# Kernel tuning notes

Measured on AMD Instinct MI355X. Metric: run time of the kernel, lower is better.

Reference implementation:

```python
import jax, jax.numpy as jnp
import numpy as np

B, L, E, K = 64, 1024, 256, 8  # batch, seq_len, d_model, topk (slice width)


def setup_inputs() -> dict:
    key = jax.random.key(0)
    ks = jax.random.split(key, 5)
    s = 1.0 / np.sqrt(E).astype(np.float32)
    return {
        "series": jax.random.normal(ks[0], (B, L, E), jnp.float32),
        "text_series": jax.random.normal(ks[1], (B, L, E), jnp.float32),
        "Wq": jax.random.normal(ks[2], (E, E), jnp.float32) * s,
        "bq": jnp.zeros((E,), jnp.float32),
        "Wk": jax.random.normal(ks[3], (E, E), jnp.float32) * s,
        "bk": jnp.zeros((E,), jnp.float32),
        "Wv": jax.random.normal(ks[4], (E, E), jnp.float32) * s,
        "bv": jnp.zeros((E,), jnp.float32),
    }


def reference(series, text_series, Wq, bq, Wk, bk, Wv, bv):
    Bn, Ln, En = series.shape
    scale = 1.0 / np.sqrt(En).astype(np.float32)
    # nn.Linear: x @ W.T + b
    q = series @ Wq.T + bq            # (B, L, E)
    k = text_series @ Wk.T + bk       # (B, L, E)
    v = text_series @ Wv.T + bv       # (B, L, E)
    # FFT cross-correlation along time axis
    qf = jnp.fft.rfft(q.transpose(0, 2, 1), axis=-1)  # (B, E, L//2+1)
    kf = jnp.fft.rfft(k.transpose(0, 2, 1), axis=-1)
    corr = jnp.fft.irfft(qf * jnp.conj(kf), n=Ln, axis=-1)  # (B, E, L)
    mean_value = corr.mean(axis=1)                           # (B, L)
    # torch.topk(mean over batch, seq_len) == full descending sort of lags
    idx = jnp.argsort(-mean_value.mean(axis=0))              # (L,)
    weights = mean_value[:, idx]                             # (B, L), sorted by lag score
    tmp_corr = jax.nn.softmax(weights * scale, axis=-1)      # (B, L)
    # Original builds cc = concat_i [roll(v, -idx[i], 1) * tmp_corr[:, i]] over all L lags
    # (shape (B, L, L*E)), then returns (cc[..., :K], cc[..., -K:]).
    # With K <= E those slices come solely from the first (i=0) and last (i=L-1) lag blocks.
    out1 = jnp.roll(v, -idx[0], axis=1)[..., :K] * tmp_corr[:, 0][:, None, None]
    out2 = jnp.roll(v, -idx[-1], axis=1)[..., -K:] * tmp_corr[:, -1][:, None, None]
    return (out1, out2)
```

## Files before the change

### kernel.cpp

```cpp
#include <hip/hip_runtime.h>
#include <hip/hip_bf16.h>
#include <math.h>

#define BB 64
#define LL 1024
#define EE 256
#define KK 8
#define EPB 8
#define CHUNKS (EE/EPB)

typedef __attribute__((ext_vector_type(8))) short  bfrag;
typedef __attribute__((ext_vector_type(4))) short  short4v;
typedef __attribute__((ext_vector_type(4))) float  f32x4;

#define MT_KB 10240

#define O_MHI    ((size_t)0)
#define O_MLO    ((size_t)40960)
#define O_BVAUG  ((size_t)81920)
#define O_X      ((size_t)81984)
#define O_KPT    (O_X + (size_t)16777216)
#define O_VSUB   (O_KPT + (size_t)16777216)
#define O_MV     (O_VSUB + (size_t)1048576)
#define O_STATS  (O_MV + (size_t)65536)

__device__ __forceinline__ float2 cmulf(float2 a, float2 b) {
    return make_float2(a.x * b.x - a.y * b.y, a.x * b.y + a.y * b.x);
}

__device__ __forceinline__ int PHY(int i) { return i + (i >> 4); }

__device__ __forceinline__ void splitbf(float x, unsigned short& h, unsigned short& l) {
    __hip_bfloat16 hb = __float2bfloat16(x);
    float hf = __bfloat162float(hb);
    __hip_bfloat16 lb = __float2bfloat16(x - hf);
    h = *(unsigned short*)&hb;
    l = *(unsigned short*)&lb;
}

__device__ __forceinline__ void gload16(const unsigned short* g, unsigned short* l) {
    __builtin_amdgcn_global_load_lds(
        (const __attribute__((address_space(1))) unsigned int*)g,
        (__attribute__((address_space(3))) unsigned int*)l, 16, 0, 0);
}

__device__ __forceinline__ int slot_of(int r, int kq) { return (kq + (r >> 1)) & 3; }

__global__ __launch_bounds__(256) void build_maug(
    const float* __restrict__ Wq, const float* __restrict__ Wk,
    const float* __restrict__ Wv, const float* __restrict__ bv,
    unsigned short* __restrict__ mhiT, unsigned short* __restrict__ mloT,
    float* __restrict__ bvaug) {
    int n = blockIdx.x;
    int j = threadIdx.x;
    float acc;
    if (n < EE) {
        acc = 0.f;
        for (int e = 0; e < EE; ++e)
            acc += Wq[e * EE + n] * Wk[e * EE + j];
    } else {
        int t = n - EE;
        int c = (t < 8) ? t : (240 + t);
        acc = Wv[c * EE + j];
    }
    unsigned short h, l;
    splitbf(acc, h, l);
    const int kb = j >> 5, kq = (j >> 3) & 3;
    const size_t dst = (size_t)kb * MT_KB + n * 32 + slot_of(n, kq) * 8 + (j & 7);
    mhiT[dst] = h;
    mloT[dst] = l;
    if (n == 0 && j < 16) bvaug[j] = bv[(j < 8) ? j : (240 + j)];
}

__global__ __launch_bounds__(256) void split_T(
    const float* __restrict__ T,
    unsigned short* __restrict__ thiT, unsigned short* __restrict__ tloT) {
    const size_t g = (size_t)blockIdx.x * 256 + threadIdx.x;
    const size_t i = g * 8;
    const int s = (int)(i >> 8), k = (int)(i & 255);
    const int kb = k >> 5, kq = (k >> 3) & 3;
    const int st = s >> 6, row = s & 63;
    f32x4 v0 = *(const f32x4*)&T[i];
    f32x4 v1 = *(const f32x4*)&T[i + 4];
    short4v h0, l0, h1, l1;
#pragma unroll
    for (int j = 0; j < 4; ++j) {
        unsigned short h, l;
        splitbf(v0[j], h, l); h0[j] = (short)h; l0[j] = (short)l;
        splitbf(v1[j], h, l); h1[j] = (short)h; l1[j] = (short)l;
    }
    const size_t dst = ((size_t)(st * 8 + kb)) * 2048 + row * 32 + slot_of(row, kq) * 8;
    *(short4v*)&thiT[dst] = h0; *(short4v*)&thiT[dst + 4] = h1;
    *(short4v*)&tloT[dst] = l0; *(short4v*)&tloT[dst + 4] = l1;
}

__global__ __launch_bounds__(256) void transpose_S(
    const float* __restrict__ S, float* __restrict__ St) {
    __shared__ float tile[32][33];
    const int b = blockIdx.z;
    const int l0 = blockIdx.x * 32, e0 = blockIdx.y * 32;
    const int tx = threadIdx.x & 31, ty = threadIdx.x >> 5;
#pragma unroll
    for (int i = 0; i < 32; i += 8)
        tile[ty + i][tx] = S[((size_t)b * LL + l0 + ty + i) * EE + e0 + tx];
    __syncthreads();
#pragma unroll
    for (int i = 0; i < 32; i += 8)
        St[((size_t)b * EE + e0 + ty + i) * LL + l0 + tx] = tile[tx][ty + i];
}

__global__ __launch_bounds__(256, 3) void gemm_mfma(
    const unsigned short* __restrict__ thiT, const unsigned short* __restrict__ tloT,
    const unsigned short* __restrict__ mhiT, const unsigned short* __restrict__ mloT,
    const float* __restrict__ bvaug,
    float* __restrict__ kp_t, float* __restrict__ vsub) {
    __shared__ alignas(16) unsigned short Ah[2048];
    __shared__ alignas(16) unsigned short Al[2048];
    __shared__ alignas(16) unsigned short Bh[10240];
    __shared__ alignas(16) unsigned short Bl[10240];
    const int tid = threadIdx.x;
    const int w = tid >> 6, lane = tid & 63;
    const int lrow = lane & 15, lk = lane >> 4;
    const int st = blockIdx.x;
    const size_t s0 = (size_t)st * 64;
    const int bb = (int)(s0 >> 10), l0 = (int)(s0 & 1023);
    const int gl = w * 64 + lane;

    f32x4 acc[4][4];
    f32x4 acc2[4];
#pragma unroll
    for (int m = 0; m < 4; ++m) {
#pragma unroll
        for (int c = 0; c < 4; ++c) acc[m][c] = (f32x4){0.f, 0.f, 0.f, 0.f};
        acc2[m] = (f32x4){0.f, 0.f, 0.f, 0.f};
    }

    for (int kb = 0; kb < 8; ++kb) {
        __syncthreads();
        const unsigned short* asrcH = thiT + ((size_t)(st * 8 + kb)) * 2048;
        const unsigned short* asrcL = tloT + ((size_t)(st * 8 + kb)) * 2048;
        gload16(asrcH + gl * 8, &Ah[(size_t)w * 512]);
        gload16(asrcL + gl * 8, &Al[(size_t)w * 512]);
        const unsigned short* bsrcH = mhiT + (size_t)kb * MT_KB;
        const unsigned short* bsrcL = mloT + (size_t)kb * MT_KB;
#pragma unroll
        for (int q = 0; q < 5; ++q)
            gload16(bsrcH + q * 2048 + gl * 8, &Bh[q * 2048 + w * 512]);
#pragma unroll
        for (int q = 0; q < 5; ++q)
            gload16(bsrcL + q * 2048 + gl * 8, &Bl[q * 2048 + w * 512]);
        __syncthreads();

        bfrag ah[4], al[4];
#pragma unroll
        for (int m = 0; m < 4; ++m) {
            const int row = m * 16 + lrow;
            const int off = row * 32 + slot_of(row, lk) * 8;
            ah[m] = *(const bfrag*)&Ah[off];
            al[m] = *(const bfrag*)&Al[off];
        }
#pragma unroll
        for (int c = 0; c < 4; ++c) {
            const int n = w * 64 + c * 16 + lrow;
            const int off = n * 32 + slot_of(n, lk) * 8;
            bfrag bh = *(const bfrag*)&Bh[off];
            bfrag bl = *(const bfrag*)&Bl[off];
#pragma unroll
            for (int m = 0; m < 4; ++m) {
                acc[m][c] = __builtin_amdgcn_mfma_f32_16x16x32_bf16(ah[m], bh, acc[m][c], 0, 0, 0);
                acc[m][c] = __builtin_amdgcn_mfma_f32_16x16x32_bf16(ah[m], bl, acc[m][c], 0, 0, 0);
                acc[m][c] = __builtin_amdgcn_mfma_f32_16x16x32_bf16(al[m], bh, acc[m][c], 0, 0, 0);
            }
        }
        if (w == 0) {
            const int n = EE + lrow;
            const int off = n * 32 + slot_of(n, lk) * 8;
            bfrag bh = *(const bfrag*)&Bh[off];
            bfrag bl = *(const bfrag*)&Bl[off];
#pragma unroll
            for (int m = 0; m < 4; ++m) {
                acc2[m] = __builtin_amdgcn_mfma_f32_16x16x32_bf16(ah[m], bh, acc2[m], 0, 0, 0);
                acc2[m] = __builtin_amdgcn_mfma_f32_16x16x32_bf16(ah[m], bl, acc2[m], 0, 0, 0);
                acc2[m] = __builtin_amdgcn_mfma_f32_16x16x32_bf16(al[m], bh, acc2[m], 0, 0, 0);
            }
        }
    }
#pragma unroll
    for (int m = 0; m < 4; ++m) {
        const int srow = m * 16 + lk * 4;
#pragma unroll
        for (int c = 0; c < 4; ++c) {
            const int n = w * 64 + c * 16 + lrow;
            *(f32x4*)&kp_t[((size_t)(bb * EE + n)) * LL + l0 + srow] = acc[m][c];
        }
    }
    if (w == 0) {
        const float bvv = bvaug[lrow];
#pragma unroll
        for (int m = 0; m < 4; ++m) {
            const int srow = m * 16 + lk * 4;
#pragma unroll
            for (int j = 0; j < 4; ++j)
                vsub[(s0 + srow + j) * 16 + lrow] = acc2[m][j] + bvv;
        }
    }
}

template<bool INV>
__device__ __forceinline__ void fft1024_r4(float2* a, float2* b,
                                           const float2* __restrict__ tw, int tid) {
    float2* src = a;
    float2* dst = b;
#pragma unroll
    for (int t = 0; t < 5; ++t) {
        const int Ns = 1 << (2 * t);
        const int sh = 8 - 2 * t;
        __syncthreads();
        const int j = tid;
        const int k = j & (Ns - 1);
        float2 w1 = tw[k << sh];
        float2 w2 = tw[k << (sh + 1)];
        float2 w3 = cmulf(w1, w2);
        if (INV) { w1.y = -w1.y; w2.y = -w2.y; w3.y = -w3.y; }
        float2 a0 = src[PHY(j)];
        float2 a1 = cmulf(w1, src[PHY(j + 256)]);
        float2 a2 = cmulf(w2, src[PHY(j + 512)]);
        float2 a3 = cmulf(w3, src[PHY(j + 768)]);
        float2 t0 = make_float2(a0.x + a2.x, a0.y + a2.y);
        float2 t1 = make_float2(a0.x - a2.x, a0.y - a2.y);
        float2 t2 = make_float2(a1.x + a3.x, a1.y + a3.y);
        float2 t3 = make_float2(a1.x - a3.x, a1.y - a3.y);
        float2 u3 = INV ? make_float2(-t3.y, t3.x) : make_float2(t3.y, -t3.x);
        const int base = ((j >> (2 * t)) << (2 * t + 2)) + k;
        dst[PHY(base)]          = make_float2(t0.x + t2.x, t0.y + t2.y);
        dst[PHY(base + Ns)]     = make_float2(t1.x + u3.x, t1.y + u3.y);
        dst[PHY(base + 2 * Ns)] = make_float2(t0.x - t2.x, t0.y - t2.y);
        dst[PHY(base + 3 * Ns)] = make_float2(t1.x - u3.x, t1.y - u3.y);
        float2* tmp = src; src = dst; dst = tmp;
    }
    __syncthreads();
}

__global__ __launch_bounds__(256) void xcorr_kernel(
    float* __restrict__ St, const float* __restrict__ kp_t) {
    __shared__ float2 bufA[1088];
    __shared__ float2 bufB[1088];
    __shared__ float2 tw[512];
    const int tid = threadIdx.x;
    const int b = blockIdx.x / CHUNKS;
    const int chunk = blockIdx.x % CHUNKS;

    for (int m = tid; m < 512; m += 256) {
        float sv, cv;
        sincosf(-2.f * 3.14159265358979323846f * (float)m / 1024.f, &sv, &cv);
        tw[m] = make_float2(cv, sv);
    }
    float2 p0 = make_float2(0.f, 0.f);
    float2 p1 = make_float2(0.f, 0.f);
    float px2 = 0.f;

    const size_t base = ((size_t)b * EE + (size_t)chunk * EPB) * LL;
    for (int ee = 0; ee < EPB; ++ee) {
        const size_t rbase = base + (size_t)ee * LL;
#pragma unroll
        for (int u = 0; u < 4; ++u) {
            int l = tid + (u << 8);
            bufA[PHY(l)] = make_float2(St[rbase + l], kp_t[rbase + l]);
        }
        fft1024_r4<false>(bufA, bufB, tw, tid);
        {
            float2 A = bufB[PHY(tid)];
            float2 C = bufB[PHY((1024 - tid) & 1023)];
            p0.x += 0.5f * (A.x * C.y + A.y * C.x);
            p0.y += 0.25f * ((A.x * A.x + A.y * A.y) - (C.x * C.x + C.y * C.y));
        }
        {
            int f = tid + 256;
            float2 A = bufB[PHY(f)];
            float2 C = bufB[PHY(1024 - f)];
            p1.x += 0.5f * (A.x * C.y + A.y * C.x);
            p1.y += 0.25f * ((A.x * A.x + A.y * A.y) - (C.x * C.x + C.y * C.y));
        }
        if (tid == 0) {
            float2 A = bufB[PHY(512)];
            px2 += A.x * A.y;
        }
    }
    float2* pp = (float2*)&St[base];
    pp[tid] = p0;
    pp[tid + 256] = p1;
    if (tid == 0) pp[512] = make_float2(px2, 0.f);
}

__global__ __launch_bounds__(256) void ifft_kernel(
    const float* __restrict__ St, float* __restrict__ mv) {
    __shared__ float2 bufA[1088];
    __shared__ float2 bufB[1088];
    __shared__ float2 tw[512];
    const int tid = threadIdx.x;
    const int b = blockIdx.x;
    for (int m = tid; m < 512; m += 256) {
        float sv, cv;
        sincosf(-2.f * 3.14159265358979323846f * (float)m / 1024.f, &sv, &cv);
        tw[m] = make_float2(cv, sv);
    }
#pragma unroll
    for (int u = 0; u < 2; ++u) {
        int f = tid + (u << 8);
        float2 s = make_float2(0.f, 0.f);
        for (int c = 0; c < CHUNKS; ++c) {
            const float2* pp = (const float2*)&St[((size_t)b * EE + (size_t)c * EPB) * LL];
            float2 v = pp[f];
            s.x += v.x; s.y += v.y;
        }
        if (f == 0) s.y = 0.f;
        bufA[PHY(f)] = s;
        if (f > 0) bufA[PHY(1024 - f)] = make_float2(s.x, -s.y);
    }
    if (tid == 0) {
        float sx = 0.f;
        for (int c = 0; c < CHUNKS; ++c) {
            const float2* pp = (const float2*)&St[((size_t)b * EE + (size_t)c * EPB) * LL];
            sx += pp[512].x;
        }
        bufA[PHY(512)] = make_float2(sx, 0.f);
    }
    fft1024_r4<true>(bufA, bufB, tw, tid);
    const float sc = 1.f / (1024.f * 256.f);
#pragma unroll
    for (int u = 0; u < 4; ++u) {
        int t = tid + (u << 8);
        mv[(size_t)b * LL + t] = bufB[PHY(t)].x * sc;
    }
}

__global__ __launch_bounds__(1024) void argidx_kernel(
    const float* __restrict__ mv, int* __restrict__ istats) {
    __shared__ float smax[1024], smin[1024];
    __shared__ int imax[1024], imin[1024];
    const int t = threadIdx.x;
    float g = 0.f;
    for (int b = 0; b < BB; ++b) g += mv[(size_t)b * LL + t];
    smax[t] = g; smin[t] = g; imax[t] = t; imin[t] = t;
    __syncthreads();
    for (int s = 512; s > 0; s >>= 1) {
        if (t < s) {
            if (smax[t + s] > smax[t] ||
                (smax[t + s] == smax[t] && imax[t + s] < imax[t])) {
                smax[t] = smax[t + s]; imax[t] = imax[t + s];
            }
            if (smin[t + s] < smin[t] ||
                (smin[t + s] == smin[t] && imin[t + s] > imin[t])) {
                smin[t] = smin[t + s]; imin[t] = imin[t + s];
            }
        }
        __syncthreads();
    }
    if (t == 0) { istats[0] = imax[0]; istats[1] = imin[0]; }
}

__global__ __launch_bounds__(256) void softmax_kernel(
    const float* __restrict__ mv, const int* __restrict__ istats,
    float* __restrict__ w01) {
    __shared__ float red[256];
    const int b = blockIdx.x, t = threadIdx.x;
    const float scale = 0.0625f;
    const float* row = mv + (size_t)b * LL;
    float m = -INFINITY;
    for (int i = t; i < LL; i += 256) m = fmaxf(m, row[i]);
    red[t] = m; __syncthreads();
    for (int s = 128; s > 0; s >>= 1) {
        if (t < s) red[t] = fmaxf(red[t], red[t + s]);
        __syncthreads();
    }
    m = red[0]; __syncthreads();
    float sum = 0.f;
    for (int i = t; i < LL; i += 256) sum += expf((row[i] - m) * scale);
    red[t] = sum; __syncthreads();
    for (int s = 128; s > 0; s >>= 1) {
        if (t < s) red[t] += red[t + s];
        __syncthreads();
    }
    if (t == 0) {
        float denom = red[0];
        w01[b]      = expf((row[istats[0]] - m) * scale) / denom;
        w01[BB + b] = expf((row[istats[1]] - m) * scale) / denom;
    }
}

__global__ __launch_bounds__(256) void out_kernel(
    const float* __restrict__ vsub, const int* __restrict__ istats,
    const float* __restrict__ w01, float* __restrict__ out) {
    const int i = blockIdx.x * 256 + threadIdx.x;
    const int half = (i >= BB * LL * KK) ? 1 : 0;
    const int j = i - half * BB * LL * KK;
    const int b = j / (LL * KK);
    const int rem = j % (LL * KK);
    const int l = rem / KK, kk = rem % KK;
    const int sh = istats[half];
    const int lr = (l + sh) & (LL - 1);
    const float w = w01[half * BB + b];
    out[i] = vsub[(size_t)(b * LL + lr) * 16 + half * 8 + kk] * w;
}

extern "C" void kernel_launch(void* const* d_in, const int* in_sizes, int n_in,
                              void* d_out, int out_size, void* d_ws, size_t ws_size,
                              hipStream_t stream) {
    const float* S  = (const float*)d_in[0];
    const float* T  = (const float*)d_in[1];
    const float* Wq = (const float*)d_in[2];
    const float* Wk = (const float*)d_in[4];
    const float* Wv = (const float*)d_in[6];
    const float* bv = (const float*)d_in[7];

    float* ws    = (float*)d_ws;
    unsigned short* mhiT = (unsigned short*)(ws + O_MHI);
    unsigned short* mloT = (unsigned short*)(ws + O_MLO);
    float* bvaug = ws + O_BVAUG;
    unsigned short* thiT = (unsigned short*)(ws + O_X);
    unsigned short* tloT = (unsigned short*)(ws + O_X + 8388608);
    float* st    = ws + O_X;
    float* kp_t  = ws + O_KPT;
    float* vsub  = ws + O_VSUB;
    float* mv    = ws + O_MV;
    float* stats = ws + O_STATS;
    int*   istats = (int*)stats;
    float* w01    = stats + 8;

    build_maug<<<272, 256, 0, stream>>>(Wq, Wk, Wv, bv, mhiT, mloT, bvaug);
    split_T<<<(BB * LL * EE) / (256 * 8), 256, 0, stream>>>(T, thiT, tloT);
    gemm_mfma<<<(BB * LL) / 64, 256, 0, stream>>>(thiT, tloT, mhiT, mloT, bvaug, kp_t, vsub);
    dim3 gT(LL / 32, EE / 32, BB);
    transpose_S<<<gT, 256, 0, stream>>>(S, st);
    xcorr_kernel<<<BB * CHUNKS, 256, 0, stream>>>(st, kp_t);
    ifft_kernel<<<BB, 256, 0, stream>>>(st, mv);
    argidx_kernel<<<1, 1024, 0, stream>>>(mv, istats);
    softmax_kernel<<<BB, 256, 0, stream>>>(mv, istats, w01);
    out_kernel<<<(2 * BB * LL * KK) / 256, 256, 0, stream>>>(vsub, istats, w01, (float*)d_out);
}
```

Before: 175.4 us.

## Compute per-channel FFTs in registers with wave shuffles instead of shared memory

Replaces the shared-memory radix-4 FFT, where a 256-thread block ran one 1024-point FFT at a time with a barrier per stage, with a per-wavefront register FFT. Each lane holds 16 points, does a radix-16 step in registers, applies twiddles, then finishes with six shuffle-based butterfly stages. Each wave handles 2 channels, so the ifft reduction now sums 128 partial slabs instead of 32. This removes LDS traffic and __syncthreads, at the cost of more partial-sum global traffic, higher register pressure and many cross-lane shuffles.

```diff
diff --git a/kernel.cpp b/kernel.cpp
--- a/kernel.cpp
+++ b/kernel.cpp
@@ -6,8 +6,6 @@
 #define LL 1024
 #define EE 256
 #define KK 8
-#define EPB 8
-#define CHUNKS (EE/EPB)
 
 typedef __attribute__((ext_vector_type(8))) short  bfrag;
 typedef __attribute__((ext_vector_type(4))) short  short4v;
@@ -203,6 +201,160 @@
             for (int j = 0; j < 4; ++j)
                 vsub[(s0 + srow + j) * 16 + lrow] = acc2[m][j] + bvv;
         }
+    }
+}
+
+#define W16_1R 0.923879532511286756f
+#define W16_1I (-0.382683432365089772f)
+#define W16_2R 0.707106781186547524f
+#define W16_2I (-0.707106781186547524f)
+#define W16_3R 0.382683432365089772f
+#define W16_3I (-0.923879532511286756f)
+#define W16_4R 0.f
+#define W16_4I (-1.f)
+#define W16_6R (-0.707106781186547524f)
+#define W16_6I (-0.707106781186547524f)
+#define W16_9R (-0.923879532511286756f)
+#define W16_9I 0.382683432365089772f
+
+__global__ __launch_bounds__(256) void xcorr_kernel(
+    float* __restrict__ St, const float* __restrict__ kp_t) {
+    const int lane = threadIdx.x & 63;
+    const int wv = threadIdx.x >> 6;
+    const int b = blockIdx.x >> 5;
+    const int c8 = blockIdx.x & 31;
+    const int e0 = c8 * 8 + 2 * wv;
+
+    const int lrev = (int)(__brev((unsigned)lane) >> 26);
+    const int l0p = (int)(__brev((unsigned)((64 - lrev) & 63)) >> 26);
+
+    const int msk[6] = {32, 16, 8, 4, 2, 1};
+    float gsg[6], wer[6], wei[6];
+#pragma unroll
+    for (int s = 0; s < 6; ++s) {
+        const int m = msk[s];
+        const int hi = lane & m;
+        gsg[s] = hi ? -1.f : 1.f;
+        if (hi) {
+            float ang = -3.14159265358979323846f * (float)(lane & (m - 1)) / (float)m;
+            float sv, cv; __sincosf(ang, &sv, &cv);
+            wer[s] = cv; wei[s] = sv;
+        } else { wer[s] = 1.f; wei[s] = 0.f; }
+    }
+    float w1r, w1i;
+    { float sv, cv; __sincosf(-2.f * 3.14159265358979323846f * (float)lane / 1024.f, &sv, &cv);
+      w1r = cv; w1i = sv; }
+
+    float pr[16], pi[16];
+#pragma unroll
+    for (int k = 0; k < 16; ++k) { pr[k] = 0.f; pi[k] = 0.f; }
+
+    const size_t base = ((size_t)b * EE + e0) * LL;
+    for (int ec = 0; ec < 2; ++ec) {
+        const float* sp = St + base + (size_t)ec * LL;
+        const float* kp = kp_t + base + (size_t)ec * LL;
+        float yr[16], yi[16];
+#pragma unroll
+        for (int r = 0; r < 16; ++r) {
+            yr[r] = sp[lane + 64 * r];
+            yi[r] = kp[lane + 64 * r];
+        }
+        {
+            float zr[16], zi[16];
+#pragma unroll
+            for (int r = 0; r < 4; ++r) {
+                float t0r = yr[r] + yr[r + 8],  t0i = yi[r] + yi[r + 8];
+                float t1r = yr[r] - yr[r + 8],  t1i = yi[r] - yi[r + 8];
+                float t2r = yr[r + 4] + yr[r + 12], t2i = yi[r + 4] + yi[r + 12];
+                float t3r = yr[r + 4] - yr[r + 12], t3i = yi[r + 4] - yi[r + 12];
+                float B0r = t0r + t2r, B0i = t0i + t2i;
+                float B1r = t1r + t3i, B1i = t1i - t3r;
+                float B2r = t0r - t2r, B2i = t0i - t2i;
+                float B3r = t1r - t3i, B3i = t1i + t3r;
+                zr[r] = B0r; zi[r] = B0i;
+                if (r == 0) {
+                    zr[4] = B1r; zi[4] = B1i;
+                    zr[8] = B2r; zi[8] = B2i;
+                    zr[12] = B3r; zi[12] = B3i;
+                } else if (r == 1) {
+                    zr[5] = B1r * W16_1R - B1i * W16_1I; zi[5] = B1r * W16_1I + B1i * W16_1R;
+                    zr[9] = B2r * W16_2R - B2i * W16_2I; zi[9] = B2r * W16_2I + B2i * W16_2R;
+                    zr[13] = B3r * W16_3R - B3i * W16_3I; zi[13] = B3r * W16_3I + B3i * W16_3R;
+                } else if (r == 2) {
+                    zr[6] = B1r * W16_2R - B1i * W16_2I; zi[6] = B1r * W16_2I + B1i * W16_2R;
+                    zr[10] = B2r * W16_4R - B2i * W16_4I; zi[10] = B2r * W16_4I + B2i * W16_4R;
+                    zr[14] = B3r * W16_6R - B3i * W16_6I; zi[14] = B3r * W16_6I + B3i * W16_6R;
+                } else {
+                    zr[7] = B1r * W16_3R - B1i * W16_3I; zi[7] = B1r * W16_3I + B1i * W16_3R;
+                    zr[11] = B2r * W16_6R - B2i * W16_6I; zi[11] = B2r * W16_6I + B2i * W16_6R;
+                    zr[15] = B3r * W16_9R - B3i * W16_9I; zi[15] = B3r * W16_9I + B3i * W16_9R;
+                }
+            }
+#pragma unroll
+            for (int p = 0; p < 4; ++p) {
+                float u0r = zr[4 * p] + zr[4 * p + 2], u0i = zi[4 * p] + zi[4 * p + 2];
+                float u1r = zr[4 * p] - zr[4 * p + 2], u1i = zi[4 * p] - zi[4 * p + 2];
+                float u2r = zr[4 * p + 1] + zr[4 * p + 3], u2i = zi[4 * p + 1] + zi[4 * p + 3];
+                float u3r = zr[4 * p + 1] - zr[4 * p + 3], u3i = zi[4 * p + 1] - zi[4 * p + 3];
+                yr[p] = u0r + u2r;       yi[p] = u0i + u2i;
+                yr[4 + p] = u1r + u3i;   yi[4 + p] = u1i - u3r;
+                yr[8 + p] = u0r - u2r;   yi[8 + p] = u0i - u2i;
+                yr[12 + p] = u1r - u3i;  yi[12 + p] = u1i + u3r;
+            }
+        }
+        {
+            float cr = w1r, ci = w1i;
+#pragma unroll
+            for (int k = 1; k < 16; ++k) {
+                float tr = yr[k] * cr - yi[k] * ci;
+                yi[k] = yr[k] * ci + yi[k] * cr;
+                yr[k] = tr;
+                if (k < 15) {
+                    float nr = cr * w1r - ci * w1i;
+                    ci = cr * w1i + ci * w1r;
+                    cr = nr;
+                }
+            }
+        }
+#pragma unroll
+        for (int k = 0; k < 16; ++k) {
+            float re = yr[k], im = yi[k];
+#pragma unroll
+            for (int s = 0; s < 6; ++s) {
+                float orr = __shfl_xor(re, msk[s]);
+                float oii = __shfl_xor(im, msk[s]);
+                float tr = orr + gsg[s] * re;
+                float ti = oii + gsg[s] * im;
+                re = tr * wer[s] - ti * wei[s];
+                im = tr * wei[s] + ti * wer[s];
+            }
+            yr[k] = re; yi[k] = im;
+        }
+        {
+            const int pl = 63 - lane;
+            float cr = __shfl(yr[0], l0p), ci = __shfl(yi[0], l0p);
+            pr[0] += 0.5f * (yr[0] * ci + yi[0] * cr);
+            pi[0] += 0.25f * ((yr[0] * yr[0] + yi[0] * yi[0]) - (cr * cr + ci * ci));
+#pragma unroll
+            for (int k = 1; k < 16; ++k) {
+                float c2r = __shfl(yr[16 - k], pl), c2i = __shfl(yi[16 - k], pl);
+                pr[k] += 0.5f * (yr[k] * c2i + yi[k] * c2r);
+                pi[k] += 0.25f * ((yr[k] * yr[k] + yi[k] * yi[k]) - (c2r * c2r + c2i * c2i));
+            }
+        }
+    }
+    float* slab = St + base;
+    if (lrev < 32) {
+#pragma unroll
+        for (int k = 0; k < 16; ++k) {
+            const int f = k + 16 * lrev;
+            slab[2 * f] = pr[k];
+            slab[2 * f + 1] = pi[k];
+        }
+    }
+    if (lane == 1) {
+        slab[1024] = pr[0];
+        slab[1025] = pi[0];
     }
 }
 
@@ -241,57 +393,6 @@
     __syncthreads();
 }
 
-__global__ __launch_bounds__(256) void xcorr_kernel(
-    float* __restrict__ St, const float* __restrict__ kp_t) {
-    __shared__ float2 bufA[1088];
-    __shared__ float2 bufB[1088];
-    __shared__ float2 tw[512];
-    const int tid = threadIdx.x;
-    const int b = blockIdx.x / CHUNKS;
-    const int chunk = blockIdx.x % CHUNKS;
-
-    for (int m = tid; m < 512; m += 256) {
-        float sv, cv;
-        sincosf(-2.f * 3.14159265358979323846f * (float)m / 1024.f, &sv, &cv);
-        tw[m] = make_float2(cv, sv);
-    }
-    float2 p0 = make_float2(0.f, 0.f);
-    float2 p1 = make_float2(0.f, 0.f);
-    float px2 = 0.f;
-
-    const size_t base = ((size_t)b * EE + (size_t)chunk * EPB) * LL;
-    for (int ee = 0; ee < EPB; ++ee) {
-        const size_t rbase = base + (size_t)ee * LL;
-#pragma unroll
-        for (int u = 0; u < 4; ++u) {
-            int l = tid + (u << 8);
-            bufA[PHY(l)] = make_float2(St[rbase + l], kp_t[rbase + l]);
-        }
-        fft1024_r4<false>(bufA, bufB, tw, tid);
-        {
-            float2 A = bufB[PHY(tid)];
-            float2 C = bufB[PHY((1024 - tid) & 1023)];
-            p0.x += 0.5f * (A.x * C.y + A.y * C.x);
-            p0.y += 0.25f * ((A.x * A.x + A.y * A.y) - (C.x * C.x + C.y * C.y));
-        }
-        {
-            int f = tid + 256;
-            float2 A = bufB[PHY(f)];
-            float2 C = bufB[PHY(1024 - f)];
-            p1.x += 0.5f * (A.x * C.y + A.y * C.x);
-            p1.y += 0.25f * ((A.x * A.x + A.y * A.y) - (C.x * C.x + C.y * C.y));
-        }
-        if (tid == 0) {
-            float2 A = bufB[PHY(512)];
-            px2 += A.x * A.y;
-        }
-    }
-    float2* pp = (float2*)&St[base];
-    pp[tid] = p0;
-    pp[tid + 256] = p1;
-    if (tid == 0) pp[512] = make_float2(px2, 0.f);
-}
-
 __global__ __launch_bounds__(256) void ifft_kernel(
     const float* __restrict__ St, float* __restrict__ mv) {
     __shared__ float2 bufA[1088];
@@ -308,8 +409,8 @@
     for (int u = 0; u < 2; ++u) {
         int f = tid + (u << 8);
         float2 s = make_float2(0.f, 0.f);
-        for (int c = 0; c < CHUNKS; ++c) {
-            const float2* pp = (const float2*)&St[((size_t)b * EE + (size_t)c * EPB) * LL];
+        for (int c = 0; c < 128; ++c) {
+            const float2* pp = (const float2*)&St[((size_t)b * EE + (size_t)c * 2) * LL];
             float2 v = pp[f];
             s.x += v.x; s.y += v.y;
         }
@@ -319,8 +420,8 @@
     }
     if (tid == 0) {
         float sx = 0.f;
-        for (int c = 0; c < CHUNKS; ++c) {
-            const float2* pp = (const float2*)&St[((size_t)b * EE + (size_t)c * EPB) * LL];
+        for (int c = 0; c < 128; ++c) {
+            const float2* pp = (const float2*)&St[((size_t)b * EE + (size_t)c * 2) * LL];
             sx += pp[512].x;
         }
         bufA[PHY(512)] = make_float2(sx, 0.f);
@@ -432,7 +533,7 @@
     gemm_mfma<<<(BB * LL) / 64, 256, 0, stream>>>(thiT, tloT, mhiT, mloT, bvaug, kp_t, vsub);
     dim3 gT(LL / 32, EE / 32, BB);
     transpose_S<<<gT, 256, 0, stream>>>(S, st);
-    xcorr_kernel<<<BB * CHUNKS, 256, 0, stream>>>(st, kp_t);
+    xcorr_kernel<<<BB * 32, 256, 0, stream>>>(st, kp_t);
     ifft_kernel<<<BB, 256, 0, stream>>>(st, mv);
     argidx_kernel<<<1, 1024, 0, stream>>>(mv, istats);
     softmax_kernel<<<BB, 256, 0, stream>>>(mv, istats, w01);
```

New measurement: 193.3 us. 10.2% more time.
